# Kernel optimization log

Hardware: AMD Instinct MI355X
Metric: run time of the kernel (lower is better)

## Reference

```python
import jax, jax.numpy as jnp
import numpy as np
from jax import lax

EPS = 1e-06


def setup_inputs() -> dict:
    key = jax.random.key(0)
    B, MICS, T, F = 16, 4, 2048, 257
    x = jax.random.uniform(key, (B, MICS, T, F), dtype=jnp.float32)
    s = jnp.array([0.025], dtype=jnp.float32)
    alpha = jnp.array([0.98], dtype=jnp.float32)
    delta = jnp.array([2.0], dtype=jnp.float32)
    r = jnp.array([0.5], dtype=jnp.float32)
    return {"x": x, "s": s, "alpha": alpha, "delta": delta, "r": r}


def reference(x, s, alpha, delta, r):
    # x: [batch, mics, chans, frames]; EMA recurrence runs over dim 2 (split dim -2 in source)
    B, MICS, T, F = x.shape
    xr = x.reshape(B * MICS, T, F)
    xt = jnp.moveaxis(xr, 1, 0)  # [T, BM, F] -- scan axis first

    s0 = s[0]

    def step(carry, frame):
        m = (1.0 - s0) * carry + s0 * frame
        return m, m

    m0 = xt[0]  # first frame: M_0 = x_0 (last_state=None branch)
    _, ms = lax.scan(step, m0, xt[1:])
    M = jnp.concatenate([m0[None], ms], axis=0)  # [T, BM, F]
    M = jnp.moveaxis(M, 0, 1)  # [BM, T, F]

    # pcen nonlinearity: (x / (M+eps)^alpha + delta)^r - delta^r
    out = jnp.power(xr / jnp.power(M + EPS, alpha) + delta, r) - jnp.power(delta, r)
    return out.reshape(B, MICS, T, F)
```

## Files before the change

### kernel.cpp

```cpp
#include <hip/hip_runtime.h>
#include <hip/hip_bf16.h>


#define EPS 1e-6f

constexpr int BM = 64;
constexpr int T  = 2048;
constexpr int F  = 257;
constexpr int L  = 128;
constexpr int C  = T / L;
constexpr int H  = 256;
constexpr int NWORK = BM * C * F;

__device__ __forceinline__ float fast_exp2(float x) { return __builtin_amdgcn_exp2f(x); }
__device__ __forceinline__ float fast_log2(float x) { return __builtin_amdgcn_logf(x); }

__device__ __forceinline__ float pcen_nl(float xv, float m, float alpha,
                                         float delta, float r, float dr) {
  float inner = fmaf(xv, fast_exp2(-alpha * fast_log2(m + EPS)), delta);
  return fast_exp2(r * fast_log2(inner)) - dr;
}

__global__ __launch_bounds__(256) void pcen_fused(
    const float* __restrict__ x, const float* __restrict__ s_p,
    const float* __restrict__ alpha_p, const float* __restrict__ delta_p,
    const float* __restrict__ r_p, float* __restrict__ out) {
  int idx = blockIdx.x * 256 + threadIdx.x;

  const float s     = s_p[0];
  const float a     = 1.0f - s;
  const float alpha = alpha_p[0];
  const float delta = delta_p[0];
  const float r     = r_p[0];
  const float dr    = fast_exp2(r * fast_log2(delta));

  int bm  = idx / (C * F);
  int rem = idx - bm * (C * F);
  int c   = rem / F;
  int f   = rem - c * F;

  const size_t col = (size_t)bm * T * F + f;
  const float* xcol = x + col;
  float*       ocol = out + col;

  const int tstart = c * L;
  int t0 = tstart - H;
  if (t0 < 0) t0 = 0;

  float m;
  int t;
  if (t0 == 0) {
    m = xcol[0];
    t = 1;
    if (c == 0) ocol[0] = pcen_nl(m, m, alpha, delta, r, dr);
  } else {
    m = 0.0f;
    t = t0;
  }

  {
    const float* p = xcol + (size_t)t * F;
    #pragma unroll 8
    for (int tt = t; tt < tstart; ++tt) {
      m = fmaf(a, m, s * p[0]);
      p += F;
    }
    if (t < tstart) t = tstart;
  }

  {
    const float* p  = xcol + (size_t)t * F;
    float*       op = ocol + (size_t)t * F;
    #pragma unroll 4
    for (int tt = t; tt < tstart + L; ++tt) {
      float xv = p[0];
      m = fmaf(a, m, s * xv);
      op[0] = pcen_nl(xv, m, alpha, delta, r, dr);
      p  += F;
      op += F;
    }
  }
}

extern "C" void kernel_launch(void* const* d_in, const int* in_sizes, int n_in,
                              void* d_out, int out_size, void* d_ws, size_t ws_size,
                              hipStream_t stream) {
  const float* x     = (const float*)d_in[0];
  const float* s     = (const float*)d_in[1];
  const float* alpha = (const float*)d_in[2];
  const float* delta = (const float*)d_in[3];
  const float* r     = (const float*)d_in[4];
  float* out = (float*)d_out;

  const int blocks = NWORK / 256;
  pcen_fused<<<blocks, 256, 0, stream>>>(x, s, alpha, delta, r, out);
}
```

Baseline: 312.9 us.

## Replace halo-warmup EMA with exact two-phase chunked scan through workspace

The approximate per-chunk warm-up, which re-read 256 halo frames per 128-frame chunk, is replaced by an exact two-pass parallel scan. Phase 1 computes each 32-frame chunk's local EMA end state into workspace. Phase 2 combines the preceding chunk states using a^L and then applies the PCEN nonlinearity with nontemporal stores. Blocks now hold one 64-lane wave striding across the frequency row, which gives coalesced row reads. This removes about 2x redundant reads and makes the result exact, at the cost of reading x twice, adding a second launch, and an O(C) prefix loop per block. A fallback kernel is kept for when no workspace is available.

```diff
diff --git a/kernel.cpp b/kernel.cpp
--- a/kernel.cpp
+++ b/kernel.cpp
@@ -7,10 +7,10 @@
 constexpr int BM = 64;
 constexpr int T  = 2048;
 constexpr int F  = 257;
-constexpr int L  = 128;
+constexpr int L  = 32;
 constexpr int C  = T / L;
-constexpr int H  = 256;
-constexpr int NWORK = BM * C * F;
+constexpr int NBLK = BM * C;
+constexpr size_t MLOC_BYTES = (size_t)BM * C * F * sizeof(float);
 
 __device__ __forceinline__ float fast_exp2(float x) { return __builtin_amdgcn_exp2f(x); }
 __device__ __forceinline__ float fast_log2(float x) { return __builtin_amdgcn_logf(x); }
@@ -21,11 +21,57 @@
   return fast_exp2(r * fast_log2(inner)) - dr;
 }
 
-__global__ __launch_bounds__(256) void pcen_fused(
+__global__ __launch_bounds__(64, 4) void pcen_phase1(
+    const float* __restrict__ x, const float* __restrict__ s_p,
+    float* __restrict__ mloc) {
+  const int b  = blockIdx.x;
+  const int l  = threadIdx.x;
+  const int bm = b >> 6;
+  const int c  = b & (C - 1);
+
+  const float s = s_p[0];
+  const float a = 1.0f - s;
+
+  const float* row = x + ((size_t)bm * T + (size_t)c * L) * F;
+
+  float m0, m1, m2, m3, m4;
+  if (c == 0) {
+    m0 = row[l]; m1 = row[l + 64]; m2 = row[l + 128]; m3 = row[l + 192];
+    m4 = row[256];
+  } else {
+    m0 = m1 = m2 = m3 = m4 = 0.0f;
+  }
+
+  const float* p = row;
+  #pragma unroll 4
+  for (int t = 0; t < L; ++t) {
+    float x0 = p[l];
+    float x1 = p[l + 64];
+    float x2 = p[l + 128];
+    float x3 = p[l + 192];
+    float x4 = p[256];
+    m0 = fmaf(a, m0, s * x0);
+    m1 = fmaf(a, m1, s * x1);
+    m2 = fmaf(a, m2, s * x2);
+    m3 = fmaf(a, m3, s * x3);
+    m4 = fmaf(a, m4, s * x4);
+    p += F;
+  }
+
+  float* mp = mloc + ((size_t)bm * C + c) * F;
+  mp[l] = m0; mp[l + 64] = m1; mp[l + 128] = m2; mp[l + 192] = m3;
+  if (l == 0) mp[256] = m4;
+}
+
+__global__ __launch_bounds__(64, 4) void pcen_phase2(
     const float* __restrict__ x, const float* __restrict__ s_p,
     const float* __restrict__ alpha_p, const float* __restrict__ delta_p,
-    const float* __restrict__ r_p, float* __restrict__ out) {
-  int idx = blockIdx.x * 256 + threadIdx.x;
+    const float* __restrict__ r_p, const float* __restrict__ mloc,
+    float* __restrict__ out) {
+  const int b  = blockIdx.x;
+  const int l  = threadIdx.x;
+  const int bm = b >> 6;
+  const int c  = b & (C - 1);
 
   const float s     = s_p[0];
   const float a     = 1.0f - s;
@@ -34,51 +80,114 @@
   const float r     = r_p[0];
   const float dr    = fast_exp2(r * fast_log2(delta));
 
-  int bm  = idx / (C * F);
-  int rem = idx - bm * (C * F);
-  int c   = rem / F;
-  int f   = rem - c * F;
-
-  const size_t col = (size_t)bm * T * F + f;
-  const float* xcol = x + col;
-  float*       ocol = out + col;
-
-  const int tstart = c * L;
-  int t0 = tstart - H;
-  if (t0 < 0) t0 = 0;
-
-  float m;
-  int t;
+  float aL = a;
+  #pragma unroll
+  for (int i = 0; i < 5; ++i) aL *= aL;
+
+  const size_t rowoff = ((size_t)bm * T + (size_t)c * L) * F;
+  const float* row  = x + rowoff;
+  float*       orow = out + rowoff;
+
+  float m0, m1, m2, m3, m4;
+  if (c == 0) {
+    m0 = row[l]; m1 = row[l + 64]; m2 = row[l + 128]; m3 = row[l + 192];
+    m4 = row[256];
+  } else {
+    const float* mp = mloc + (size_t)bm * C * F;
+    m0 = mp[l]; m1 = mp[l + 64]; m2 = mp[l + 128]; m3 = mp[l + 192];
+    m4 = mp[256];
+    const float* q = mp + F;
+    #pragma unroll 2
+    for (int cc = 1; cc < c; ++cc) {
+      m0 = fmaf(aL, m0, q[l]);
+      m1 = fmaf(aL, m1, q[l + 64]);
+      m2 = fmaf(aL, m2, q[l + 128]);
+      m3 = fmaf(aL, m3, q[l + 192]);
+      m4 = fmaf(aL, m4, q[256]);
+      q += F;
+    }
+  }
+
+  const float* p  = row;
+  float*       op = orow;
+  #pragma unroll 2
+  for (int t = 0; t < L; ++t) {
+    float x0 = p[l];
+    float x1 = p[l + 64];
+    float x2 = p[l + 128];
+    float x3 = p[l + 192];
+    float x4 = p[256];
+    m0 = fmaf(a, m0, s * x0);
+    m1 = fmaf(a, m1, s * x1);
+    m2 = fmaf(a, m2, s * x2);
+    m3 = fmaf(a, m3, s * x3);
+    m4 = fmaf(a, m4, s * x4);
+    __builtin_nontemporal_store(pcen_nl(x0, m0, alpha, delta, r, dr), &op[l]);
+    __builtin_nontemporal_store(pcen_nl(x1, m1, alpha, delta, r, dr), &op[l + 64]);
+    __builtin_nontemporal_store(pcen_nl(x2, m2, alpha, delta, r, dr), &op[l + 128]);
+    __builtin_nontemporal_store(pcen_nl(x3, m3, alpha, delta, r, dr), &op[l + 192]);
+    if (l == 0)
+      __builtin_nontemporal_store(pcen_nl(x4, m4, alpha, delta, r, dr), &op[256]);
+    p  += F;
+    op += F;
+  }
+}
+
+constexpr int FB_L = 128;
+constexpr int FB_C = T / FB_L;
+constexpr int FB_H = 256;
+__global__ __launch_bounds__(64, 4) void pcen_fallback(
+    const float* __restrict__ x, const float* __restrict__ s_p,
+    const float* __restrict__ alpha_p, const float* __restrict__ delta_p,
+    const float* __restrict__ r_p, float* __restrict__ out) {
+  const int b  = blockIdx.x;
+  const int l  = threadIdx.x;
+  const int bm = b / FB_C;
+  const int c  = b % FB_C;
+
+  const float s     = s_p[0];
+  const float a     = 1.0f - s;
+  const float alpha = alpha_p[0];
+  const float delta = delta_p[0];
+  const float r     = r_p[0];
+  const float dr    = fast_exp2(r * fast_log2(delta));
+
+  const size_t colbase = (size_t)bm * T * F;
+  const int tstart = c * FB_L;
+  int t0 = tstart - FB_H; if (t0 < 0) t0 = 0;
+
+  float m0, m1, m2, m3, m4;
+  const float* row0 = x + colbase + (size_t)t0 * F;
   if (t0 == 0) {
-    m = xcol[0];
-    t = 1;
-    if (c == 0) ocol[0] = pcen_nl(m, m, alpha, delta, r, dr);
-  } else {
-    m = 0.0f;
-    t = t0;
-  }
-
-  {
-    const float* p = xcol + (size_t)t * F;
-    #pragma unroll 8
-    for (int tt = t; tt < tstart; ++tt) {
-      m = fmaf(a, m, s * p[0]);
-      p += F;
-    }
-    if (t < tstart) t = tstart;
-  }
-
-  {
-    const float* p  = xcol + (size_t)t * F;
-    float*       op = ocol + (size_t)t * F;
-    #pragma unroll 4
-    for (int tt = t; tt < tstart + L; ++tt) {
-      float xv = p[0];
-      m = fmaf(a, m, s * xv);
-      op[0] = pcen_nl(xv, m, alpha, delta, r, dr);
-      p  += F;
-      op += F;
-    }
+    m0 = row0[l]; m1 = row0[l + 64]; m2 = row0[l + 128]; m3 = row0[l + 192];
+    m4 = row0[256];
+  } else {
+    m0 = m1 = m2 = m3 = m4 = 0.0f;
+  }
+
+  const float* p = row0;
+  for (int t = t0; t < tstart; ++t) {
+    float x0 = p[l], x1 = p[l + 64], x2 = p[l + 128], x3 = p[l + 192], x4 = p[256];
+    m0 = fmaf(a, m0, s * x0); m1 = fmaf(a, m1, s * x1);
+    m2 = fmaf(a, m2, s * x2); m3 = fmaf(a, m3, s * x3);
+    m4 = fmaf(a, m4, s * x4);
+    p += F;
+  }
+  p = x + colbase + (size_t)tstart * F;
+  float* op = out + colbase + (size_t)tstart * F;
+  for (int t = 0; t < FB_L; ++t) {
+    float x0 = p[l], x1 = p[l + 64], x2 = p[l + 128], x3 = p[l + 192], x4 = p[256];
+    m0 = fmaf(a, m0, s * x0); m1 = fmaf(a, m1, s * x1);
+    m2 = fmaf(a, m2, s * x2); m3 = fmaf(a, m3, s * x3);
+    m4 = fmaf(a, m4, s * x4);
+    __builtin_nontemporal_store(pcen_nl(x0, m0, alpha, delta, r, dr), &op[l]);
+    __builtin_nontemporal_store(pcen_nl(x1, m1, alpha, delta, r, dr), &op[l + 64]);
+    __builtin_nontemporal_store(pcen_nl(x2, m2, alpha, delta, r, dr), &op[l + 128]);
+    __builtin_nontemporal_store(pcen_nl(x3, m3, alpha, delta, r, dr), &op[l + 192]);
+    if (l == 0)
+      __builtin_nontemporal_store(pcen_nl(x4, m4, alpha, delta, r, dr), &op[256]);
+    p  += F;
+    op += F;
   }
 }
 
@@ -92,6 +201,11 @@
   const float* r     = (const float*)d_in[4];
   float* out = (float*)d_out;
 
-  const int blocks = NWORK / 256;
-  pcen_fused<<<blocks, 256, 0, stream>>>(x, s, alpha, delta, r, out);
-}
+  if (d_ws != nullptr && ws_size >= MLOC_BYTES) {
+    float* mloc = (float*)d_ws;
+    pcen_phase1<<<NBLK, 64, 0, stream>>>(x, s, mloc);
+    pcen_phase2<<<NBLK, 64, 0, stream>>>(x, s, alpha, delta, r, mloc, out);
+  } else {
+    pcen_fallback<<<BM * FB_C, 64, 0, stream>>>(x, s, alpha, delta, r, out);
+  }
+}
```

Measured after the change: 301.0 us. 3.8% less time.
